# Kernel tuning notes

Measured on AMD Instinct MI355X. Metric: run time of the kernel, lower is better.

Reference implementation:

```python
import jax, jax.numpy as jnp
import numpy as np

N_NODES = 100_000
N_EDGES = 1_600_000
N_GRAPHS = 512
NODE_TYPE_BUCKETS = 256
IDENT_BUCKETS = 50_000
NODE_EMB = 64
IDENT_EMB = 32
IN_DIM = NODE_EMB + IDENT_EMB + 6  # 102
HID = 128
NUM_CATS = 10


def setup_inputs() -> dict:
    key = jax.random.key(0)
    ks = jax.random.split(key, 24)
    p = lambda k, shp: (jax.random.normal(k, shp, dtype=jnp.float32) * 0.05)
    return {
        "node_type_ids": jax.random.randint(ks[0], (N_NODES,), 0, NODE_TYPE_BUCKETS + 2),
        "ident_hash_ids": jax.random.randint(ks[1], (N_NODES,), 0, IDENT_BUCKETS + 2),
        "literal_flags": jax.random.uniform(ks[2], (N_NODES, 5), dtype=jnp.float32),
        "node_depth": jax.random.randint(ks[3], (N_NODES,), 0, 60),
        "edge_index": jax.random.randint(ks[4], (2, N_EDGES), 0, N_NODES),
        "batch_index": jnp.sort(jax.random.randint(ks[5], (N_NODES,), 0, N_GRAPHS)),
        "emb_node": p(ks[6], (NODE_TYPE_BUCKETS + 2, NODE_EMB)),
        "emb_ident": p(ks[7], (IDENT_BUCKETS + 2, IDENT_EMB)),
        "W_self0": p(ks[8], (IN_DIM, HID)), "b_self0": p(ks[9], (HID,)),
        "W_neigh0": p(ks[10], (IN_DIM, HID)), "b_neigh0": p(ks[11], (HID,)),
        "W_self1": p(ks[12], (HID, HID)), "b_self1": p(ks[13], (HID,)),
        "W_neigh1": p(ks[14], (HID, HID)), "b_neigh1": p(ks[15], (HID,)),
        "W_risk": p(ks[16], (HID, 1)), "b_risk": p(ks[17], (1,)),
        "W_cat": p(ks[18], (HID, NUM_CATS)), "b_cat": p(ks[19], (NUM_CATS,)),
    }


def reference(node_type_ids, ident_hash_ids, literal_flags, node_depth,
              edge_index, batch_index, emb_node, emb_ident,
              W_self0, b_self0, W_neigh0, b_neigh0,
              W_self1, b_self1, W_neigh1, b_neigh1,
              W_risk, b_risk, W_cat, b_cat):
    n = node_type_ids.shape[0]
    # node features: [N, 64+32+5+1]
    depth = node_depth.astype(jnp.float32)[:, None]
    depth = depth / jnp.maximum(depth.max(), 1.0)
    x = jnp.concatenate([emb_node[node_type_ids], emb_ident[ident_hash_ids],
                         literal_flags, depth], axis=-1)
    src, dst = edge_index[0], edge_index[1]
    # in-degree, shared across layers (clamped to 1)
    deg = jax.ops.segment_sum(jnp.ones_like(dst, jnp.float32), dst, num_segments=n)
    inv_deg = (1.0 / jnp.maximum(deg, 1.0))[:, None]

    def sage(x, Ws, bs, Wn, bn):
        agg = jax.ops.segment_sum(x[src], dst, num_segments=n)  # gather+scatter-sum
        neigh = agg * inv_deg
        return jax.nn.relu(x @ Ws + bs + neigh @ Wn + bn)

    x = sage(x, W_self0, b_self0, W_neigh0, b_neigh0)
    x = sage(x, W_self1, b_self1, W_neigh1, b_neigh1)

    # global mean pool over graphs
    pooled = jax.ops.segment_sum(x, batch_index, num_segments=N_GRAPHS)
    counts = jax.ops.segment_sum(jnp.ones((n,), jnp.float32), batch_index,
                                 num_segments=N_GRAPHS)
    g = pooled / jnp.maximum(counts, 1.0)[:, None]

    risk_logit = (g @ W_risk + b_risk)[:, 0]
    category_logits = g @ W_cat + b_cat
    return risk_logit, category_logits
```

## Files before the change

kernel.cpp:

```cpp
#include <hip/hip_runtime.h>
#include <cstdint>
#include <cstddef>

#define HIDDIM 128
#define NGRAPH_MAX 512
#define LDSPAD 136
#define NBKT_MAX 512

using short8 = __attribute__((ext_vector_type(8))) short;
using f32x4  = __attribute__((ext_vector_type(4))) float;

__device__ __forceinline__ unsigned short f2bf(float x) {
    union { float f; uint32_t u; } v; v.f = x;
    uint32_t r = v.u + 0x7fffu + ((v.u >> 16) & 1u);
    return (unsigned short)(r >> 16);
}
__device__ __forceinline__ float bf2f(unsigned short h) {
    union { uint32_t u; float f; } v; v.u = ((uint32_t)h) << 16;
    return v.f;
}
__device__ __forceinline__ float bflo(uint32_t u) { return __uint_as_float(u << 16); }
__device__ __forceinline__ float bfhi(uint32_t u) { return __uint_as_float(u & 0xffff0000u); }

__global__ void k_bcount(const int* __restrict__ dst, int* __restrict__ bcount, int E) {
    __shared__ int hist[NBKT_MAX];
    int t = threadIdx.x;
    hist[t] = 0; hist[t + 256] = 0;
    __syncthreads();
    int c0 = blockIdx.x * 4096;
    int ce = min(4096, E - c0);
    for (int i = t; i < ce; i += 256)
        atomicAdd(&hist[dst[c0 + i] >> 8], 1);
    __syncthreads();
    for (int b = t; b < NBKT_MAX; b += 256)
        if (hist[b]) atomicAdd(&bcount[b], hist[b]);
}

__global__ void k_bscan(const int* __restrict__ bcount, int* __restrict__ boff,
                        int* __restrict__ bcur, int* __restrict__ rowptr,
                        int nbkt, int N, int E) {
    __shared__ int sd[512];
    int t = threadIdx.x;
    int v = (t < nbkt) ? bcount[t] : 0;
    sd[t] = v;
    __syncthreads();
    for (int off = 1; off < 512; off <<= 1) {
        int x = (t >= off) ? sd[t - off] : 0;
        __syncthreads();
        sd[t] += x;
        __syncthreads();
    }
    if (t < nbkt) { boff[t] = sd[t] - v; bcur[t] = sd[t] - v; }
    if (t == 0) { boff[nbkt] = E; rowptr[N] = E; }
}

__global__ void k_bscatter(const int* __restrict__ src, const int* __restrict__ dst,
                           int* __restrict__ bcur, int2* __restrict__ ebuf, int E, int nbkt) {
    __shared__ int2 stage[4096];
    __shared__ int hist[NBKT_MAX];
    __shared__ int ofs[NBKT_MAX];
    __shared__ int cur[NBKT_MAX];
    __shared__ int gbase[NBKT_MAX];
    __shared__ int scanbuf[256];
    int t = threadIdx.x;
    int c0 = blockIdx.x * 4096;
    int ce = min(4096, E - c0);

    hist[t] = 0; hist[t + 256] = 0;
    __syncthreads();
    for (int i = t; i < ce; i += 256)
        atomicAdd(&hist[dst[c0 + i] >> 8], 1);
    __syncthreads();
    int h2a = hist[2 * t], h2b = hist[2 * t + 1];
    int ps = h2a + h2b;
    scanbuf[t] = ps;
    __syncthreads();
    for (int off = 1; off < 256; off <<= 1) {
        int x = (t >= off) ? scanbuf[t - off] : 0;
        __syncthreads();
        scanbuf[t] += x;
        __syncthreads();
    }
    int ex = scanbuf[t] - ps;
    ofs[2 * t] = ex;           cur[2 * t] = ex;
    ofs[2 * t + 1] = ex + h2a; cur[2 * t + 1] = ex + h2a;
    __syncthreads();
    for (int i = t; i < ce; i += 256) {
        int d = dst[c0 + i];
        int p = atomicAdd(&cur[d >> 8], 1);
        stage[p] = make_int2(src[c0 + i], d);
    }
    __syncthreads();
    for (int b = t; b < nbkt; b += 256) {
        int c = hist[b];
        gbase[b] = c ? atomicAdd(&bcur[b], c) : 0;
    }
    __syncthreads();
    for (int j = t; j < ce; j += 256) {
        int2 p = stage[j];
        int b = p.y >> 8;
        ebuf[gbase[b] + (j - ofs[b])] = p;
    }
}

__global__ void k_build(const int2* __restrict__ ebuf, const int* __restrict__ boff,
                        int* __restrict__ rowptr, float* __restrict__ invd,
                        int* __restrict__ srcs, int N) {
    __shared__ int ldeg[256];
    __shared__ int lofs[256];
    __shared__ int lcur[256];
    int b = blockIdx.x, t = threadIdx.x;
    int n0 = b << 8;
    int s = boff[b], e = boff[b + 1];
    ldeg[t] = 0;
    __syncthreads();
    for (int i = s + t; i < e; i += 256)
        atomicAdd(&ldeg[ebuf[i].y & 255], 1);
    __syncthreads();
    int v = ldeg[t];
    lofs[t] = v;
    __syncthreads();
    for (int off = 1; off < 256; off <<= 1) {
        int x = (t >= off) ? lofs[t - off] : 0;
        __syncthreads();
        lofs[t] += x;
        __syncthreads();
    }
    int excl = lofs[t] - v;
    int node = n0 + t;
    if (node < N) {
        rowptr[node] = s + excl;
        invd[node] = 1.0f / (float)max(v, 1);
    }
    lcur[t] = excl;
    __syncthreads();
    for (int i = s + t; i < e; i += 256) {
        int2 p = ebuf[i];
        int slot = atomicAdd(&lcur[p.y & 255], 1);
        srcs[s + slot] = p.x;
    }
}

__global__ void k_nodestats(const int* __restrict__ batch, const int* __restrict__ depth,
                            int* __restrict__ counts, int* __restrict__ maxd, int N, int G) {
    __shared__ int hist[NGRAPH_MAX];
    __shared__ int red[256];
    int t = threadIdx.x;
    for (int b = t; b < G; b += 256) hist[b] = 0;
    __syncthreads();
    int i = blockIdx.x * 256 + t;
    int d = 0;
    if (i < N) {
        atomicAdd(&hist[batch[i]], 1);
        d = depth[i];
    }
    red[t] = d;
    __syncthreads();
    for (int off = 128; off > 0; off >>= 1) {
        if (t < off) red[t] = max(red[t], red[t + off]);
        __syncthreads();
    }
    if (t == 0) atomicMax(maxd, red[0]);
    for (int b = t; b < G; b += 256)
        if (hist[b]) atomicAdd(&counts[b], hist[b]);
}

__global__ void k_feat(const int* __restrict__ nt, const int* __restrict__ ih,
                       const float* __restrict__ flags, const int* __restrict__ depth,
                       const float* __restrict__ embN, const float* __restrict__ embI,
                       const int* __restrict__ maxd, unsigned short* __restrict__ x0, int N) {
    int idx = blockIdx.x * 256 + threadIdx.x;
    int i = idx >> 7;
    int f = idx & 127;
    if (i >= N) return;
    float v;
    if (f < 64)       v = embN[nt[i] * 64 + f];
    else if (f < 96)  v = embI[ih[i] * 32 + (f - 64)];
    else if (f < 101) v = flags[i * 5 + (f - 96)];
    else if (f == 101) {
        float md = fmaxf((float)(*maxd), 1.0f);
        v = (float)depth[i] / md;
    } else v = 0.0f;
    x0[(size_t)i * HIDDIM + f] = f2bf(v);
}

__global__ void k_wt(const float* __restrict__ Wn0, const float* __restrict__ Ws0,
                     const float* __restrict__ Wn1, const float* __restrict__ Ws1,
                     int K0, unsigned short* __restrict__ Wt) {
    int b = blockIdx.x;
    int mat = b >> 7, n = b & 127, t = threadIdx.x;
    const float* W = (mat == 0) ? Wn0 : (mat == 1) ? Ws0 : (mat == 2) ? Wn1 : Ws1;
    int K = (mat < 2) ? K0 : HIDDIM;
    Wt[(size_t)mat * HIDDIM * HIDDIM + n * HIDDIM + t] =
        (t < K) ? f2bf(W[(size_t)t * HIDDIM + n]) : (unsigned short)0;
}

__global__ __launch_bounds__(256, 1) void k_gemm2(
    const unsigned short* __restrict__ X,
    const unsigned short* __restrict__ Wtn, const unsigned short* __restrict__ Wts,
    int N, const float* __restrict__ bias_s, const float* __restrict__ bias_n,
    unsigned short* __restrict__ Y, unsigned short* __restrict__ S) {
    __shared__ unsigned short As[128 * LDSPAD];
    __shared__ unsigned short Bn[128 * LDSPAD];
    __shared__ unsigned short Bs[128 * LDSPAD];
    int t = threadIdx.x;
    int rowBase = blockIdx.x << 7;

    #pragma unroll
    for (int it = 0; it < 8; it++) {
        int idx = t + it * 256;
        int r = idx >> 4, seg = idx & 15;
        int gr = rowBase + r;
        uint4 v = make_uint4(0u, 0u, 0u, 0u);
        if (gr < N) v = *(const uint4*)(X + (size_t)gr * HIDDIM + seg * 8);
        *(uint4*)&As[r * LDSPAD + seg * 8] = v;
    }
    #pragma unroll
    for (int it = 0; it < 8; it++) {
        int idx = t + it * 256;
        int n = idx >> 4, seg = idx & 15;
        *(uint4*)&Bn[n * LDSPAD + seg * 8] = *(const uint4*)(Wtn + n * HIDDIM + seg * 8);
        *(uint4*)&Bs[n * LDSPAD + seg * 8] = *(const uint4*)(Wts + n * HIDDIM + seg * 8);
    }
    __syncthreads();

    int lane = t & 63;
    int wv = t >> 6;
    int ml = lane & 15;
    int quad = lane >> 4;
    int m0 = wv * 32;

    f32x4 accY[2][8], accS[2][8];
    #pragma unroll
    for (int i = 0; i < 2; i++)
        #pragma unroll
        for (int j = 0; j < 8; j++) {
            accY[i][j] = (f32x4){0.f, 0.f, 0.f, 0.f};
            accS[i][j] = (f32x4){0.f, 0.f, 0.f, 0.f};
        }

    #pragma unroll
    for (int kt = 0; kt < 4; kt++) {
        int ko = kt * 32 + quad * 8;
        short8 a0 = *(const short8*)&As[(m0 + ml) * LDSPAD + ko];
        short8 a1 = *(const short8*)&As[(m0 + 16 + ml) * LDSPAD + ko];
        #pragma unroll
        for (int nt = 0; nt < 8; nt++) {
            short8 bn = *(const short8*)&Bn[(nt * 16 + ml) * LDSPAD + ko];
            accY[0][nt] = __builtin_amdgcn_mfma_f32_16x16x32_bf16(a0, bn, accY[0][nt], 0, 0, 0);
            accY[1][nt] = __builtin_amdgcn_mfma_f32_16x16x32_bf16(a1, bn, accY[1][nt], 0, 0, 0);
            short8 bs = *(const short8*)&Bs[(nt * 16 + ml) * LDSPAD + ko];
            accS[0][nt] = __builtin_amdgcn_mfma_f32_16x16x32_bf16(a0, bs, accS[0][nt], 0, 0, 0);
            accS[1][nt] = __builtin_amdgcn_mfma_f32_16x16x32_bf16(a1, bs, accS[1][nt], 0, 0, 0);
        }
    }

    float bsum[8];
    #pragma unroll
    for (int nt = 0; nt < 8; nt++) {
        int col = nt * 16 + ml;
        bsum[nt] = bias_s[col] + bias_n[col];
    }

    #pragma unroll
    for (int mt = 0; mt < 2; mt++) {
        int grow0 = rowBase + m0 + mt * 16 + quad * 4;
        #pragma unroll
        for (int r = 0; r < 4; r++) {
            int grow = grow0 + r;
            if (grow >= N) continue;
            #pragma unroll
            for (int nt = 0; nt < 8; nt++) {
                int col = nt * 16 + ml;
                Y[(size_t)grow * HIDDIM + col] = f2bf(accY[mt][nt][r]);
                S[(size_t)grow * HIDDIM + col] = f2bf(accS[mt][nt][r] + bsum[nt]);
            }
        }
    }
}

__global__ void k_aggc(const uint32_t* __restrict__ y, const uint32_t* __restrict__ s2,
                       const int* __restrict__ rp, const int* __restrict__ srcs,
                       const float* __restrict__ invd, uint32_t* __restrict__ xo, int N) {
    int t = threadIdx.x;
    int lane = t & 63;
    int half = lane >> 5;
    int cl = lane & 31;
    int d = blockIdx.x * 4 + (t >> 6);
    if (d >= N) return;
    int s = rp[d], e = rp[d + 1];
    const uint2* y2 = (const uint2*)y;
    float a0 = 0.f, a1 = 0.f, a2 = 0.f, a3 = 0.f;
    for (int base = s; base < e; base += 64) {
        int m = min(64, e - base);
        int idx = (lane < m) ? srcs[base + lane] : 0;
        int j = 0;
        for (; j + 8 <= m; j += 8) {
            int i0 = __shfl(idx, j + 0 + half, 64);
            int i1 = __shfl(idx, j + 2 + half, 64);
            int i2 = __shfl(idx, j + 4 + half, 64);
            int i3 = __shfl(idx, j + 6 + half, 64);
            uint2 u0 = y2[(size_t)i0 * 32 + cl];
            uint2 u1 = y2[(size_t)i1 * 32 + cl];
            uint2 u2 = y2[(size_t)i2 * 32 + cl];
            uint2 u3 = y2[(size_t)i3 * 32 + cl];
            a0 += bflo(u0.x); a1 += bfhi(u0.x); a2 += bflo(u0.y); a3 += bfhi(u0.y);
            a0 += bflo(u1.x); a1 += bfhi(u1.x); a2 += bflo(u1.y); a3 += bfhi(u1.y);
            a0 += bflo(u2.x); a1 += bfhi(u2.x); a2 += bflo(u2.y); a3 += bfhi(u2.y);
            a0 += bflo(u3.x); a1 += bfhi(u3.x); a2 += bflo(u3.y); a3 += bfhi(u3.y);
        }
        for (; j + 2 <= m; j += 2) {
            int id = __shfl(idx, j + half, 64);
            uint2 u = y2[(size_t)id * 32 + cl];
            a0 += bflo(u.x); a1 += bfhi(u.x); a2 += bflo(u.y); a3 += bfhi(u.y);
        }
        if (j < m) {
            int id = __shfl(idx, j, 64);
            if (half == 0) {
                uint2 u = y2[(size_t)id * 32 + cl];
                a0 += bflo(u.x); a1 += bfhi(u.x); a2 += bflo(u.y); a3 += bfhi(u.y);
            }
        }
    }
    a0 += __shfl_down(a0, 32, 64);
    a1 += __shfl_down(a1, 32, 64);
    a2 += __shfl_down(a2, 32, 64);
    a3 += __shfl_down(a3, 32, 64);
    if (half == 0) {
        float iv = invd[d];
        uint2 su = ((const uint2*)s2)[(size_t)d * 32 + cl];
        float o0 = fmaxf(bflo(su.x) + a0 * iv, 0.f);
        float o1 = fmaxf(bfhi(su.x) + a1 * iv, 0.f);
        float o2 = fmaxf(bflo(su.y) + a2 * iv, 0.f);
        float o3 = fmaxf(bfhi(su.y) + a3 * iv, 0.f);
        uint2 o;
        o.x = (uint32_t)f2bf(o0) | ((uint32_t)f2bf(o1) << 16);
        o.y = (uint32_t)f2bf(o2) | ((uint32_t)f2bf(o3) << 16);
        ((uint2*)xo)[(size_t)d * 32 + cl] = o;
    }
}

__global__ void k_scang(const int* __restrict__ counts, int* __restrict__ gstart, int G) {
    __shared__ int sd[NGRAPH_MAX];
    int t = threadIdx.x;
    int v = (t < G) ? counts[t] : 0;
    sd[t] = v;
    __syncthreads();
    for (int off = 1; off < 512; off <<= 1) {
        int x = (t >= off) ? sd[t - off] : 0;
        __syncthreads();
        sd[t] += x;
        __syncthreads();
    }
    if (t < G) gstart[t] = sd[t] - v;
    if (t == G - 1) gstart[G] = sd[t];
}

__global__ void k_pool(const uint32_t* __restrict__ x, const int* __restrict__ gstart,
                       const int* __restrict__ counts, float* __restrict__ g) {
    __shared__ float red[3][128];
    int gr = blockIdx.x, t = threadIdx.x;
    int wv = t >> 6, lane = t & 63;
    int half = lane >> 5, cl = lane & 31;
    int s = gstart[gr], e = gstart[gr + 1];
    const uint2* x2 = (const uint2*)x;
    float a0 = 0.f, a1 = 0.f, a2 = 0.f, a3 = 0.f;
    for (int r0 = s + wv * 2 + half; r0 < e; r0 += 32) {
        uint2 u0 = x2[(size_t)r0 * 32 + cl];
        int r1 = r0 + 8, r2 = r0 + 16, r3 = r0 + 24;
        uint2 u1 = make_uint2(0u, 0u), u2 = make_uint2(0u, 0u), u3 = make_uint2(0u, 0u);
        if (r1 < e) u1 = x2[(size_t)r1 * 32 + cl];
        if (r2 < e) u2 = x2[(size_t)r2 * 32 + cl];
        if (r3 < e) u3 = x2[(size_t)r3 * 32 + cl];
        a0 += bflo(u0.x); a1 += bfhi(u0.x); a2 += bflo(u0.y); a3 += bfhi(u0.y);
        a0 += bflo(u1.x); a1 += bfhi(u1.x); a2 += bflo(u1.y); a3 += bfhi(u1.y);
        a0 += bflo(u2.x); a1 += bfhi(u2.x); a2 += bflo(u2.y); a3 += bfhi(u2.y);
        a0 += bflo(u3.x); a1 += bfhi(u3.x); a2 += bflo(u3.y); a3 += bfhi(u3.y);
    }
    a0 += __shfl_down(a0, 32, 64);
    a1 += __shfl_down(a1, 32, 64);
    a2 += __shfl_down(a2, 32, 64);
    a3 += __shfl_down(a3, 32, 64);
    if (half == 0 && wv > 0) {
        red[wv - 1][cl * 4 + 0] = a0;
        red[wv - 1][cl * 4 + 1] = a1;
        red[wv - 1][cl * 4 + 2] = a2;
        red[wv - 1][cl * 4 + 3] = a3;
    }
    __syncthreads();
    if (wv == 0 && half == 0) {
        a0 += red[0][cl * 4 + 0] + red[1][cl * 4 + 0] + red[2][cl * 4 + 0];
        a1 += red[0][cl * 4 + 1] + red[1][cl * 4 + 1] + red[2][cl * 4 + 1];
        a2 += red[0][cl * 4 + 2] + red[1][cl * 4 + 2] + red[2][cl * 4 + 2];
        a3 += red[0][cl * 4 + 3] + red[1][cl * 4 + 3] + red[2][cl * 4 + 3];
        float inv = 1.0f / fmaxf((float)counts[gr], 1.0f);
        float4 o = make_float4(a0 * inv, a1 * inv, a2 * inv, a3 * inv);
        *(float4*)&g[(size_t)gr * HIDDIM + cl * 4] = o;
    }
}

__global__ void k_head(const float* __restrict__ g, const float* __restrict__ Wr,
                       const float* __restrict__ br, const float* __restrict__ Wc,
                       const float* __restrict__ bc, float* __restrict__ out, int G) {
    __shared__ float row[128];
    int gr = blockIdx.x;
    int t = threadIdx.x;
    row[t] = g[(size_t)gr * HIDDIM + t];
    __syncthreads();
    if (t == 0) {
        float s = 0.f;
        for (int k = 0; k < 128; k++) s += row[k] * Wr[k];
        out[gr] = s + br[0];
    } else if (t <= 10) {
        int j = t - 1;
        float s = 0.f;
        for (int k = 0; k < 128; k++) s += row[k] * Wc[k * 10 + j];
        out[G + gr * 10 + j] = s + bc[j];
    }
}

extern "C" void kernel_launch(void* const* d_in, const int* in_sizes, int n_in,
                              void* d_out, int out_size, void* d_ws, size_t ws_size,
                              hipStream_t stream) {
    const int*   nt    = (const int*)d_in[0];
    const int*   ih    = (const int*)d_in[1];
    const float* flags = (const float*)d_in[2];
    const int*   depth = (const int*)d_in[3];
    const int*   eidx  = (const int*)d_in[4];
    const int*   batch = (const int*)d_in[5];
    const float* embN  = (const float*)d_in[6];
    const float* embI  = (const float*)d_in[7];
    const float* Ws0   = (const float*)d_in[8];
    const float* bs0   = (const float*)d_in[9];
    const float* Wn0   = (const float*)d_in[10];
    const float* bn0   = (const float*)d_in[11];
    const float* Ws1   = (const float*)d_in[12];
    const float* bs1   = (const float*)d_in[13];
    const float* Wn1   = (const float*)d_in[14];
    const float* bn1   = (const float*)d_in[15];
    const float* Wr    = (const float*)d_in[16];
    const float* br    = (const float*)d_in[17];
    const float* Wc    = (const float*)d_in[18];
    const float* bc    = (const float*)d_in[19];
    float* out = (float*)d_out;

    const int N  = in_sizes[0];
    const int E  = in_sizes[4] / 2;
    const int K0 = in_sizes[8] / HIDDIM;
    const int G  = out_size / 11;
    const int* esrc = eidx;
    const int* edst = eidx + E;
    const int NBKT = (N + 255) >> 8;

    char* w = (char*)d_ws;
    const size_t NH = (size_t)N * HIDDIM * sizeof(unsigned short);
    unsigned short* bufA = (unsigned short*)(w);
    unsigned short* bufY = (unsigned short*)(w + NH);
    unsigned short* bufS = (unsigned short*)(w + 2 * NH);
    unsigned short* bufX1= (unsigned short*)(w + 3 * NH);
    char* p = w + 4 * NH;
    unsigned short* Wt = (unsigned short*)p; p += (size_t)4 * HIDDIM * HIDDIM * 2;
    int2* ebuf  = (int2*)p;          p += (size_t)E * 8;
    int* srcs   = (int*)p;           p += (size_t)E * 4;
    int* rowptr = (int*)p;           p += (size_t)(N + 1) * 4;
    float* invd = (float*)p;         p += (size_t)N * 4;
    int* gstart = (int*)p;           p += (size_t)(G + 1) * 4;
    float* gmat = (float*)p;         p += (size_t)G * HIDDIM * 4;
    int* boff   = (int*)p;           p += (size_t)(NBKT_MAX + 1) * 4;
    int* bcur   = (int*)p;           p += (size_t)NBKT_MAX * 4;
    int* bcount = (int*)p;           p += (size_t)NBKT_MAX * 4;
    int* counts = (int*)p;           p += (size_t)G * 4;
    int* maxd   = (int*)p;           p += 4;
    const size_t zero_bytes = (size_t)(NBKT_MAX + G + 1) * 4;
    (void)n_in; (void)ws_size;

    const int nbC = (E + 4095) / 4096;
    const int nbN = (N + 255) / 256;
    const int nbF = ((size_t)N * HIDDIM + 255) / 256;
    const int nbG = (N + 127) / 128;
    const int nbA = (N + 3) / 4;

    hipMemsetAsync(bcount, 0, zero_bytes, stream);

    k_bcount<<<nbC, 256, 0, stream>>>(edst, bcount, E);
    k_nodestats<<<nbN, 256, 0, stream>>>(batch, depth, counts, maxd, N, G);
    k_wt<<<512, 128, 0, stream>>>(Wn0, Ws0, Wn1, Ws1, K0, Wt);
    k_bscan<<<1, 512, 0, stream>>>(bcount, boff, bcur, rowptr, NBKT, N, E);
    k_bscatter<<<nbC, 256, 0, stream>>>(esrc, edst, bcur, ebuf, E, NBKT);
    k_build<<<NBKT, 256, 0, stream>>>(ebuf, boff, rowptr, invd, srcs, N);

    k_feat<<<nbF, 256, 0, stream>>>(nt, ih, flags, depth, embN, embI, maxd, bufA, N);

    const unsigned short* Wt_n0 = Wt;
    const unsigned short* Wt_s0 = Wt + 1 * HIDDIM * HIDDIM;
    const unsigned short* Wt_n1 = Wt + 2 * HIDDIM * HIDDIM;
    const unsigned short* Wt_s1 = Wt + 3 * HIDDIM * HIDDIM;

    k_gemm2<<<nbG, 256, 0, stream>>>(bufA, Wt_n0, Wt_s0, N, bs0, bn0, bufY, bufS);
    k_aggc<<<nbA, 256, 0, stream>>>((const uint32_t*)bufY, (const uint32_t*)bufS,
                                    rowptr, srcs, invd, (uint32_t*)bufX1, N);

    k_gemm2<<<nbG, 256, 0, stream>>>(bufX1, Wt_n1, Wt_s1, N, bs1, bn1, bufY, bufS);
    k_aggc<<<nbA, 256, 0, stream>>>((const uint32_t*)bufY, (const uint32_t*)bufS,
                                    rowptr, srcs, invd, (uint32_t*)bufA, N);

    k_scang<<<1, 512, 0, stream>>>(counts, gstart, G);
    k_pool<<<G, 256, 0, stream>>>((const uint32_t*)bufA, gstart, counts, gmat);
    k_head<<<G, 128, 0, stream>>>(gmat, Wr, br, Wc, bc, out, G);
}
```

Measured before the change: 404.0 us.

## Merge preprocessing kernels, fuse pool with head, read GEMM weights from global

```diff
diff --git a/kernel.cpp b/kernel.cpp
--- a/kernel.cpp
+++ b/kernel.cpp
@@ -22,36 +22,110 @@
 __device__ __forceinline__ float bflo(uint32_t u) { return __uint_as_float(u << 16); }
 __device__ __forceinline__ float bfhi(uint32_t u) { return __uint_as_float(u & 0xffff0000u); }
 
-__global__ void k_bcount(const int* __restrict__ dst, int* __restrict__ bcount, int E) {
+__global__ void k_prep(const int* __restrict__ nt, const int* __restrict__ ih,
+                       const float* __restrict__ flags, const int* __restrict__ depth,
+                       const float* __restrict__ embN, const float* __restrict__ embI,
+                       const int* __restrict__ edst, const int* __restrict__ batch,
+                       const float* __restrict__ Wn0, const float* __restrict__ Ws0,
+                       const float* __restrict__ Wn1, const float* __restrict__ Ws1,
+                       int K0, int N, int E, int G,
+                       unsigned short* __restrict__ x0, unsigned short* __restrict__ Wt,
+                       int* __restrict__ bcount, int* __restrict__ counts,
+                       int* __restrict__ maxd,
+                       int nbF, int nbC, int nbN) {
     __shared__ int hist[NBKT_MAX];
-    int t = threadIdx.x;
-    hist[t] = 0; hist[t + 256] = 0;
-    __syncthreads();
-    int c0 = blockIdx.x * 4096;
-    int ce = min(4096, E - c0);
-    for (int i = t; i < ce; i += 256)
-        atomicAdd(&hist[dst[c0 + i] >> 8], 1);
-    __syncthreads();
-    for (int b = t; b < NBKT_MAX; b += 256)
-        if (hist[b]) atomicAdd(&bcount[b], hist[b]);
-}
-
-__global__ void k_bscan(const int* __restrict__ bcount, int* __restrict__ boff,
-                        int* __restrict__ bcur, int* __restrict__ rowptr,
-                        int nbkt, int N, int E) {
+    __shared__ int red[256];
+    int b = blockIdx.x, t = threadIdx.x;
+    if (b < nbF) {
+        int idx = b * 256 + t;
+        int i = idx >> 7;
+        int f = idx & 127;
+        if (i >= N) return;
+        float v;
+        if (f < 64)       v = embN[nt[i] * 64 + f];
+        else if (f < 96)  v = embI[ih[i] * 32 + (f - 64)];
+        else if (f < 101) v = flags[i * 5 + (f - 96)];
+        else v = 0.0f;
+        x0[(size_t)i * HIDDIM + f] = f2bf(v);
+    } else if (b < nbF + nbC) {
+        hist[t] = 0; hist[t + 256] = 0;
+        __syncthreads();
+        int c0 = (b - nbF) * 4096;
+        int ce = min(4096, E - c0);
+        for (int i = t; i < ce; i += 256)
+            atomicAdd(&hist[edst[c0 + i] >> 8], 1);
+        __syncthreads();
+        for (int bb = t; bb < NBKT_MAX; bb += 256)
+            if (hist[bb]) atomicAdd(&bcount[bb], hist[bb]);
+    } else if (b < nbF + nbC + nbN) {
+        for (int g = t; g < G; g += 256) hist[g] = 0;
+        __syncthreads();
+        int i = (b - nbF - nbC) * 256 + t;
+        int d = 0;
+        if (i < N) {
+            atomicAdd(&hist[batch[i]], 1);
+            d = depth[i];
+        }
+        red[t] = d;
+        __syncthreads();
+        for (int off = 128; off > 0; off >>= 1) {
+            if (t < off) red[t] = max(red[t], red[t + off]);
+            __syncthreads();
+        }
+        if (t == 0) atomicMax(maxd, red[0]);
+        for (int g = t; g < G; g += 256)
+            if (hist[g]) atomicAdd(&counts[g], hist[g]);
+    } else {
+        int idx = (b - nbF - nbC - nbN) * 256 + t;
+        int mat = idx >> 14;
+        int rem = idx & 16383;
+        int n = rem >> 7, k = rem & 127;
+        const float* W = (mat == 0) ? Wn0 : (mat == 1) ? Ws0 : (mat == 2) ? Wn1 : Ws1;
+        int K = (mat < 2) ? K0 : HIDDIM;
+        Wt[(size_t)mat * HIDDIM * HIDDIM + n * HIDDIM + k] =
+            (k < K) ? f2bf(W[(size_t)k * HIDDIM + n]) : (unsigned short)0;
+    }
+}
+
+__global__ void k_scan2x(const int* __restrict__ bcount, int* __restrict__ boff,
+                         int* __restrict__ bcur, int* __restrict__ rowptr,
+                         const int* __restrict__ counts, int* __restrict__ gstart,
+                         const int* __restrict__ depth, const int* __restrict__ maxd,
+                         unsigned short* __restrict__ x0,
+                         int nbkt, int N, int E, int G) {
     __shared__ int sd[512];
-    int t = threadIdx.x;
-    int v = (t < nbkt) ? bcount[t] : 0;
-    sd[t] = v;
-    __syncthreads();
-    for (int off = 1; off < 512; off <<= 1) {
-        int x = (t >= off) ? sd[t - off] : 0;
-        __syncthreads();
-        sd[t] += x;
-        __syncthreads();
-    }
-    if (t < nbkt) { boff[t] = sd[t] - v; bcur[t] = sd[t] - v; }
-    if (t == 0) { boff[nbkt] = E; rowptr[N] = E; }
+    int b = blockIdx.x, t = threadIdx.x;
+    if (b == 0) {
+        int v = (t < nbkt) ? bcount[t] : 0;
+        sd[t] = v;
+        __syncthreads();
+        for (int off = 1; off < 512; off <<= 1) {
+            int x = (t >= off) ? sd[t - off] : 0;
+            __syncthreads();
+            sd[t] += x;
+            __syncthreads();
+        }
+        if (t < nbkt) { boff[t] = sd[t] - v; bcur[t] = sd[t] - v; }
+        if (t == 0) { boff[nbkt] = E; rowptr[N] = E; }
+    } else if (b == 1) {
+        int v = (t < G) ? counts[t] : 0;
+        sd[t] = v;
+        __syncthreads();
+        for (int off = 1; off < 512; off <<= 1) {
+            int x = (t >= off) ? sd[t - off] : 0;
+            __syncthreads();
+            sd[t] += x;
+            __syncthreads();
+        }
+        if (t < G) gstart[t] = sd[t] - v;
+        if (t == G - 1) gstart[G] = sd[t];
+    } else {
+        int i = (b - 2) * 512 + t;
+        if (i < N) {
+            float md = fmaxf((float)(*maxd), 1.0f);
+            x0[(size_t)i * HIDDIM + 101] = f2bf((float)depth[i] / md);
+        }
+    }
 }
 
 __global__ void k_bscatter(const int* __restrict__ src, const int* __restrict__ dst,
@@ -141,68 +215,12 @@
     }
 }
 
-__global__ void k_nodestats(const int* __restrict__ batch, const int* __restrict__ depth,
-                            int* __restrict__ counts, int* __restrict__ maxd, int N, int G) {
-    __shared__ int hist[NGRAPH_MAX];
-    __shared__ int red[256];
-    int t = threadIdx.x;
-    for (int b = t; b < G; b += 256) hist[b] = 0;
-    __syncthreads();
-    int i = blockIdx.x * 256 + t;
-    int d = 0;
-    if (i < N) {
-        atomicAdd(&hist[batch[i]], 1);
-        d = depth[i];
-    }
-    red[t] = d;
-    __syncthreads();
-    for (int off = 128; off > 0; off >>= 1) {
-        if (t < off) red[t] = max(red[t], red[t + off]);
-        __syncthreads();
-    }
-    if (t == 0) atomicMax(maxd, red[0]);
-    for (int b = t; b < G; b += 256)
-        if (hist[b]) atomicAdd(&counts[b], hist[b]);
-}
-
-__global__ void k_feat(const int* __restrict__ nt, const int* __restrict__ ih,
-                       const float* __restrict__ flags, const int* __restrict__ depth,
-                       const float* __restrict__ embN, const float* __restrict__ embI,
-                       const int* __restrict__ maxd, unsigned short* __restrict__ x0, int N) {
-    int idx = blockIdx.x * 256 + threadIdx.x;
-    int i = idx >> 7;
-    int f = idx & 127;
-    if (i >= N) return;
-    float v;
-    if (f < 64)       v = embN[nt[i] * 64 + f];
-    else if (f < 96)  v = embI[ih[i] * 32 + (f - 64)];
-    else if (f < 101) v = flags[i * 5 + (f - 96)];
-    else if (f == 101) {
-        float md = fmaxf((float)(*maxd), 1.0f);
-        v = (float)depth[i] / md;
-    } else v = 0.0f;
-    x0[(size_t)i * HIDDIM + f] = f2bf(v);
-}
-
-__global__ void k_wt(const float* __restrict__ Wn0, const float* __restrict__ Ws0,
-                     const float* __restrict__ Wn1, const float* __restrict__ Ws1,
-                     int K0, unsigned short* __restrict__ Wt) {
-    int b = blockIdx.x;
-    int mat = b >> 7, n = b & 127, t = threadIdx.x;
-    const float* W = (mat == 0) ? Wn0 : (mat == 1) ? Ws0 : (mat == 2) ? Wn1 : Ws1;
-    int K = (mat < 2) ? K0 : HIDDIM;
-    Wt[(size_t)mat * HIDDIM * HIDDIM + n * HIDDIM + t] =
-        (t < K) ? f2bf(W[(size_t)t * HIDDIM + n]) : (unsigned short)0;
-}
-
-__global__ __launch_bounds__(256, 1) void k_gemm2(
+__global__ __launch_bounds__(256, 3) void k_gemm2(
     const unsigned short* __restrict__ X,
     const unsigned short* __restrict__ Wtn, const unsigned short* __restrict__ Wts,
     int N, const float* __restrict__ bias_s, const float* __restrict__ bias_n,
     unsigned short* __restrict__ Y, unsigned short* __restrict__ S) {
     __shared__ unsigned short As[128 * LDSPAD];
-    __shared__ unsigned short Bn[128 * LDSPAD];
-    __shared__ unsigned short Bs[128 * LDSPAD];
     int t = threadIdx.x;
     int rowBase = blockIdx.x << 7;
 
@@ -215,13 +233,6 @@
         if (gr < N) v = *(const uint4*)(X + (size_t)gr * HIDDIM + seg * 8);
         *(uint4*)&As[r * LDSPAD + seg * 8] = v;
     }
-    #pragma unroll
-    for (int it = 0; it < 8; it++) {
-        int idx = t + it * 256;
-        int n = idx >> 4, seg = idx & 15;
-        *(uint4*)&Bn[n * LDSPAD + seg * 8] = *(const uint4*)(Wtn + n * HIDDIM + seg * 8);
-        *(uint4*)&Bs[n * LDSPAD + seg * 8] = *(const uint4*)(Wts + n * HIDDIM + seg * 8);
-    }
     __syncthreads();
 
     int lane = t & 63;
@@ -246,10 +257,11 @@
         short8 a1 = *(const short8*)&As[(m0 + 16 + ml) * LDSPAD + ko];
         #pragma unroll
         for (int nt = 0; nt < 8; nt++) {
-            short8 bn = *(const short8*)&Bn[(nt * 16 + ml) * LDSPAD + ko];
+            int boffs = (nt * 16 + ml) * HIDDIM + ko;
+            short8 bn = *(const short8*)&Wtn[boffs];
+            short8 bs = *(const short8*)&Wts[boffs];
             accY[0][nt] = __builtin_amdgcn_mfma_f32_16x16x32_bf16(a0, bn, accY[0][nt], 0, 0, 0);
             accY[1][nt] = __builtin_amdgcn_mfma_f32_16x16x32_bf16(a1, bn, accY[1][nt], 0, 0, 0);
-            short8 bs = *(const short8*)&Bs[(nt * 16 + ml) * LDSPAD + ko];
             accS[0][nt] = __builtin_amdgcn_mfma_f32_16x16x32_bf16(a0, bs, accS[0][nt], 0, 0, 0);
             accS[1][nt] = __builtin_amdgcn_mfma_f32_16x16x32_bf16(a1, bs, accS[1][nt], 0, 0, 0);
         }
@@ -340,25 +352,13 @@
     }
 }
 
-__global__ void k_scang(const int* __restrict__ counts, int* __restrict__ gstart, int G) {
-    __shared__ int sd[NGRAPH_MAX];
-    int t = threadIdx.x;
-    int v = (t < G) ? counts[t] : 0;
-    sd[t] = v;
-    __syncthreads();
-    for (int off = 1; off < 512; off <<= 1) {
-        int x = (t >= off) ? sd[t - off] : 0;
-        __syncthreads();
-        sd[t] += x;
-        __syncthreads();
-    }
-    if (t < G) gstart[t] = sd[t] - v;
-    if (t == G - 1) gstart[G] = sd[t];
-}
-
-__global__ void k_pool(const uint32_t* __restrict__ x, const int* __restrict__ gstart,
-                       const int* __restrict__ counts, float* __restrict__ g) {
+__global__ void k_poolhead(const uint32_t* __restrict__ x, const int* __restrict__ gstart,
+                           const int* __restrict__ counts,
+                           const float* __restrict__ Wr, const float* __restrict__ br,
+                           const float* __restrict__ Wc, const float* __restrict__ bc,
+                           float* __restrict__ out, int G) {
     __shared__ float red[3][128];
+    __shared__ float rowf[128];
     int gr = blockIdx.x, t = threadIdx.x;
     int wv = t >> 6, lane = t & 63;
     int half = lane >> 5, cl = lane & 31;
@@ -394,28 +394,21 @@
         a2 += red[0][cl * 4 + 2] + red[1][cl * 4 + 2] + red[2][cl * 4 + 2];
         a3 += red[0][cl * 4 + 3] + red[1][cl * 4 + 3] + red[2][cl * 4 + 3];
         float inv = 1.0f / fmaxf((float)counts[gr], 1.0f);
-        float4 o = make_float4(a0 * inv, a1 * inv, a2 * inv, a3 * inv);
-        *(float4*)&g[(size_t)gr * HIDDIM + cl * 4] = o;
-    }
-}
-
-__global__ void k_head(const float* __restrict__ g, const float* __restrict__ Wr,
-                       const float* __restrict__ br, const float* __restrict__ Wc,
-                       const float* __restrict__ bc, float* __restrict__ out, int G) {
-    __shared__ float row[128];
-    int gr = blockIdx.x;
-    int t = threadIdx.x;
-    row[t] = g[(size_t)gr * HIDDIM + t];
+        rowf[cl * 4 + 0] = a0 * inv;
+        rowf[cl * 4 + 1] = a1 * inv;
+        rowf[cl * 4 + 2] = a2 * inv;
+        rowf[cl * 4 + 3] = a3 * inv;
+    }
     __syncthreads();
     if (t == 0) {
-        float s = 0.f;
-        for (int k = 0; k < 128; k++) s += row[k] * Wr[k];
-        out[gr] = s + br[0];
+        float s2 = 0.f;
+        for (int k = 0; k < 128; k++) s2 += rowf[k] * Wr[k];
+        out[gr] = s2 + br[0];
     } else if (t <= 10) {
         int j = t - 1;
-        float s = 0.f;
-        for (int k = 0; k < 128; k++) s += row[k] * Wc[k * 10 + j];
-        out[G + gr * 10 + j] = s + bc[j];
+        float s2 = 0.f;
+        for (int k = 0; k < 128; k++) s2 += rowf[k] * Wc[k * 10 + j];
+        out[G + gr * 10 + j] = s2 + bc[j];
     }
 }
 
@@ -465,7 +458,6 @@
     int* rowptr = (int*)p;           p += (size_t)(N + 1) * 4;
     float* invd = (float*)p;         p += (size_t)N * 4;
     int* gstart = (int*)p;           p += (size_t)(G + 1) * 4;
-    float* gmat = (float*)p;         p += (size_t)G * HIDDIM * 4;
     int* boff   = (int*)p;           p += (size_t)(NBKT_MAX + 1) * 4;
     int* bcur   = (int*)p;           p += (size_t)NBKT_MAX * 4;
     int* bcount = (int*)p;           p += (size_t)NBKT_MAX * 4;
@@ -479,17 +471,21 @@
     const int nbF = ((size_t)N * HIDDIM + 255) / 256;
     const int nbG = (N + 127) / 128;
     const int nbA = (N + 3) / 4;
+    const int nbD = (N + 511) / 512;
 
     hipMemsetAsync(bcount, 0, zero_bytes, stream);
 
-    k_bcount<<<nbC, 256, 0, stream>>>(edst, bcount, E);
-    k_nodestats<<<nbN, 256, 0, stream>>>(batch, depth, counts, maxd, N, G);
-    k_wt<<<512, 128, 0, stream>>>(Wn0, Ws0, Wn1, Ws1, K0, Wt);
-    k_bscan<<<1, 512, 0, stream>>>(bcount, boff, bcur, rowptr, NBKT, N, E);
+    k_prep<<<nbF + nbC + nbN + 256, 256, 0, stream>>>(
+        nt, ih, flags, depth, embN, embI, edst, batch,
+        Wn0, Ws0, Wn1, Ws1, K0, N, E, G,
+        bufA, Wt, bcount, counts, maxd, nbF, nbC, nbN);
+
+    k_scan2x<<<2 + nbD, 512, 0, stream>>>(bcount, boff, bcur, rowptr,
+                                          counts, gstart, depth, maxd, bufA,
+                                          NBKT, N, E, G);
+
     k_bscatter<<<nbC, 256, 0, stream>>>(esrc, edst, bcur, ebuf, E, NBKT);
     k_build<<<NBKT, 256, 0, stream>>>(ebuf, boff, rowptr, invd, srcs, N);
-
-    k_feat<<<nbF, 256, 0, stream>>>(nt, ih, flags, depth, embN, embI, maxd, bufA, N);
 
     const unsigned short* Wt_n0 = Wt;
     const unsigned short* Wt_s0 = Wt + 1 * HIDDIM * HIDDIM;
@@ -504,7 +500,6 @@
     k_aggc<<<nbA, 256, 0, stream>>>((const uint32_t*)bufY, (const uint32_t*)bufS,
                                     rowptr, srcs, invd, (uint32_t*)bufA, N);
 
-    k_scang<<<1, 512, 0, stream>>>(counts, gstart, G);
-    k_pool<<<G, 256, 0, stream>>>((const uint32_t*)bufA, gstart, counts, gmat);
-    k_head<<<G, 128, 0, stream>>>(gmat, Wr, br, Wc, bc, out, G);
-}
+    k_poolhead<<<G, 256, 0, stream>>>((const uint32_t*)bufA, gstart, counts,
+                                      Wr, br, Wc, bc, out, G);
+}
```

Result: slower. 460.8 us (+14.1%).
